# Performance work log

Hardware: AMD Instinct MI355X
Metric: run time of the kernel (lower is better)

The kernel has to match this reference:

```python
import jax, jax.numpy as jnp
import numpy as np

N = 50000      # nodes
E = 800000     # edges (before self loops)
EMB = 128      # input feature dim
HID = 32       # per-head hidden dim
HEADS = 4      # gat1 heads
G = 64         # graphs in batch
NEG_SLOPE = 0.2


def setup_inputs() -> dict:
    key = jax.random.key(0)
    ks = jax.random.split(key, 14)
    glorot = lambda k, shape, fan: (jax.random.normal(k, shape) / np.sqrt(fan)).astype(jnp.float32)
    x = jax.random.normal(ks[0], (N, EMB), dtype=jnp.float32)
    edge_index = jax.random.randint(ks[1], (2, E), 0, N, dtype=jnp.int64)
    batch = jnp.sort(jax.random.randint(ks[2], (N,), 0, G, dtype=jnp.int64))
    return {
        "x": x,
        "edge_index": edge_index,
        "batch": batch,
        # GATConv 1: EMB -> HID per head, HEADS heads, concat
        "W1": glorot(ks[3], (EMB, HEADS * HID), EMB),
        "att_src1": glorot(ks[4], (HEADS, HID), HID),
        "att_dst1": glorot(ks[5], (HEADS, HID), HID),
        "b1": jnp.zeros((HEADS * HID,), jnp.float32),
        # GATConv 2: HEADS*HID -> HID, 1 head
        "W2": glorot(ks[6], (HEADS * HID, HID), HEADS * HID),
        "att_src2": glorot(ks[7], (1, HID), HID),
        "att_dst2": glorot(ks[8], (1, HID), HID),
        "b2": jnp.zeros((HID,), jnp.float32),
        # attentional pooling gate MLP: Linear(HID,HID)->ReLU->Linear(HID,1)
        "g_w1": glorot(ks[9], (HID, HID), HID),
        "g_b1": jnp.zeros((HID,), jnp.float32),
        "g_w2": glorot(ks[10], (HID, 1), HID),
        "g_b2": jnp.zeros((1,), jnp.float32),
    }


def _gat(x, W, att_src, att_dst, bias, src, dst, heads, out_dim):
    """PyG-style GATConv with precomputed self-looped (src, dst)."""
    n = x.shape[0]
    h = (x @ W).reshape(n, heads, out_dim)              # [N, H, C]
    a_src = (h * att_src).sum(-1)                       # [N, H]
    a_dst = (h * att_dst).sum(-1)                       # [N, H]
    e = jax.nn.leaky_relu(a_src[src] + a_dst[dst], NEG_SLOPE)   # [Etot, H]
    # segment softmax over incoming edges of each dst node
    m = jax.ops.segment_max(e, dst, num_segments=n)
    ex = jnp.exp(e - m[dst])
    denom = jax.ops.segment_sum(ex, dst, num_segments=n)
    alpha = ex / (denom[dst] + 1e-16)                   # [Etot, H]
    out = jax.ops.segment_sum(alpha[:, :, None] * h[src], dst, num_segments=n)
    return out.reshape(n, heads * out_dim) + bias


def reference(x, edge_index, batch, W1, att_src1, att_dst1, b1,
              W2, att_src2, att_dst2, b2, g_w1, g_b1, g_w2, g_b2):
    n = x.shape[0]
    loops = jnp.arange(n, dtype=edge_index.dtype)
    src = jnp.concatenate([edge_index[0], loops])       # add_self_loops=True
    dst = jnp.concatenate([edge_index[1], loops])
    h = jax.nn.elu(_gat(x, W1, att_src1, att_dst1, b1, src, dst, HEADS, HID))
    h = jax.nn.elu(_gat(h, W2, att_src2, att_dst2, b2, src, dst, 1, HID))
    # attentional aggregation per graph
    gate = jax.nn.relu(h @ g_w1 + g_b1) @ g_w2 + g_b2   # [N, 1]
    gm = jax.ops.segment_max(gate, batch, num_segments=G)
    ge = jnp.exp(gate - gm[batch])
    gs = jax.ops.segment_sum(ge, batch, num_segments=G)
    w = ge / (gs[batch] + 1e-16)
    return jax.ops.segment_sum(w * h, batch, num_segments=G)  # [G, HID]
```

## Files before the change

kernel.cpp:

```cpp
#include <hip/hip_runtime.h>
#include <hip/hip_bf16.h>

#define NEG_SLOPE 0.2f
#define BW  128
#define BSH 7

__device__ __forceinline__ float elu1f(float v) {
    return v > 0.f ? v : expm1f(v);
}
__device__ __forceinline__ float bf2f(ushort u) {
    return __uint_as_float(((unsigned)u) << 16);
}
__device__ __forceinline__ ushort f2bf(float f) {
    return __bfloat16_as_ushort(__float2bfloat16(f));
}
__device__ __forceinline__ unsigned fflip(float f) {
    unsigned u = __float_as_uint(f);
    return (u & 0x80000000u) ? ~u : (u | 0x80000000u);
}
__device__ __forceinline__ float funflip(unsigned u) {
    u = (u & 0x80000000u) ? (u & 0x7FFFFFFFu) : ~u;
    return __uint_as_float(u);
}

__global__ __launch_bounds__(256) void k_bcount(
    const int* __restrict__ ei, int E, int Et, int nbk, int* __restrict__ bcnt)
{
    __shared__ int h[512];
    for (int i = threadIdx.x; i < nbk; i += 256) h[i] = 0;
    __syncthreads();
    const int start = blockIdx.x * 4096;
    const int end   = min(start + 4096, Et);
    for (int i = start + threadIdx.x; i < end; i += 256) {
        int d = (i < E) ? ei[E + i] : i - E;
        atomicAdd(&h[d >> BSH], 1);
    }
    __syncthreads();
    for (int i = threadIdx.x; i < nbk; i += 256)
        if (h[i]) atomicAdd(&bcnt[i], h[i]);
}

__global__ __launch_bounds__(512) void k_bscan(
    const int* __restrict__ bcnt, int nbk, int Et,
    int* __restrict__ bbase, int* __restrict__ bcur)
{
    __shared__ int s[512];
    int v = (threadIdx.x < nbk) ? bcnt[threadIdx.x] : 0;
    s[threadIdx.x] = v;
    __syncthreads();
#pragma unroll
    for (int off = 1; off < 512; off <<= 1) {
        int t = (threadIdx.x >= off) ? s[threadIdx.x - off] : 0;
        __syncthreads();
        s[threadIdx.x] += t;
        __syncthreads();
    }
    if (threadIdx.x < nbk) {
        int ex = s[threadIdx.x] - v;
        bbase[threadIdx.x] = ex;
        bcur[threadIdx.x]  = ex;
    }
    if (threadIdx.x == 0) bbase[nbk] = Et;
}

__global__ __launch_bounds__(256) void k_bscatter(
    const int* __restrict__ ei, int E, int Et, int nbk,
    int* __restrict__ bcur, int2* __restrict__ ebuk)
{
    __shared__ int h[512];
    __shared__ int cur[512];
    for (int i = threadIdx.x; i < nbk; i += 256) h[i] = 0;
    __syncthreads();
    const int start = blockIdx.x * 4096;
    const int end   = min(start + 4096, Et);
    for (int i = start + threadIdx.x; i < end; i += 256) {
        int d = (i < E) ? ei[E + i] : i - E;
        atomicAdd(&h[d >> BSH], 1);
    }
    __syncthreads();
    for (int i = threadIdx.x; i < nbk; i += 256)
        cur[i] = h[i] ? atomicAdd(&bcur[i], h[i]) : 0;
    __syncthreads();
    for (int i = start + threadIdx.x; i < end; i += 256) {
        int s, d;
        if (i < E) { s = ei[i]; d = ei[E + i]; } else { s = i - E; d = s; }
        int p = atomicAdd(&cur[d >> BSH], 1);
        ebuk[p] = make_int2(s, d);
    }
}

__global__ __launch_bounds__(256) void k_bdeg(
    const int2* __restrict__ ebuk, const int* __restrict__ bbase,
    int N, int* __restrict__ deg)
{
    const int b = blockIdx.x;
    __shared__ int cnt[BW];
    if (threadIdx.x < BW) cnt[threadIdx.x] = 0;
    __syncthreads();
    const int d0 = b << BSH;
    const int e0 = bbase[b], e1 = bbase[b + 1];
    for (int i = e0 + threadIdx.x; i < e1; i += 256)
        atomicAdd(&cnt[ebuk[i].y - d0], 1);
    __syncthreads();
    if (threadIdx.x < BW) {
        int d = d0 + threadIdx.x;
        if (d < N) deg[d] = cnt[threadIdx.x];
    }
}

__global__ __launch_bounds__(256) void k_fine(
    const int2* __restrict__ ebuk, const int* __restrict__ bbase,
    const int* __restrict__ rowp, int N, int* __restrict__ esrc)
{
    const int b = blockIdx.x;
    __shared__ int lcur[BW];
    const int d0 = b << BSH;
    if (threadIdx.x < BW) {
        int d = d0 + threadIdx.x;
        lcur[threadIdx.x] = (d < N) ? rowp[d] : 0;
    }
    __syncthreads();
    const int e0 = bbase[b], e1 = bbase[b + 1];
    for (int i = e0 + threadIdx.x; i < e1; i += 256) {
        int2 e = ebuk[i];
        int p = atomicAdd(&lcur[e.y - d0], 1);
        esrc[p] = e.x;
    }
}

__global__ __launch_bounds__(256) void k_scan1(const int* __restrict__ deg, int N,
                                               int* __restrict__ row, int* __restrict__ bsum)
{
    __shared__ int s[256];
    int i = blockIdx.x * 256 + threadIdx.x;
    int v = (i < N) ? deg[i] : 0;
    s[threadIdx.x] = v;
    __syncthreads();
#pragma unroll
    for (int off = 1; off < 256; off <<= 1) {
        int t = (threadIdx.x >= off) ? s[threadIdx.x - off] : 0;
        __syncthreads();
        s[threadIdx.x] += t;
        __syncthreads();
    }
    if (i < N) row[i] = s[threadIdx.x] - v;
    if (threadIdx.x == 255) bsum[blockIdx.x] = s[255];
}

__global__ __launch_bounds__(256) void k_scan2(int* __restrict__ bsum, int nb)
{
    __shared__ int s[256];
    int v = (threadIdx.x < nb) ? bsum[threadIdx.x] : 0;
    s[threadIdx.x] = v;
    __syncthreads();
#pragma unroll
    for (int off = 1; off < 256; off <<= 1) {
        int t = (threadIdx.x >= off) ? s[threadIdx.x - off] : 0;
        __syncthreads();
        s[threadIdx.x] += t;
        __syncthreads();
    }
    if (threadIdx.x < nb) bsum[threadIdx.x] = s[threadIdx.x] - v;
}

__global__ void k_scan3(int* __restrict__ row, const int* __restrict__ bsum, int N, int Et)
{
    int i = blockIdx.x * 256 + threadIdx.x;
    if (i < N) row[i] += bsum[blockIdx.x];
    if (i == 0) row[N] = Et;
}

template <int H>
__global__ __launch_bounds__(256) void k_redmax(const unsigned* __restrict__ in, int nblk,
                                                float* __restrict__ out)
{
    __shared__ unsigned sm[H];
    if (threadIdx.x < H) sm[threadIdx.x] = 0;
    __syncthreads();
    unsigned m[H];
#pragma unroll
    for (int h = 0; h < H; h++) m[h] = 0;
    for (int i = threadIdx.x; i < nblk; i += 256) {
#pragma unroll
        for (int h = 0; h < H; h++) m[h] = max(m[h], in[i * H + h]);
    }
#pragma unroll
    for (int h = 0; h < H; h++) atomicMax(&sm[h], m[h]);
    __syncthreads();
    if (threadIdx.x < H) out[threadIdx.x] = funflip(sm[threadIdx.x]);
}

__global__ __launch_bounds__(256) void k_gemm1(
    const float* __restrict__ x, const float* __restrict__ W,
    const float* __restrict__ att_s, const float* __restrict__ att_d,
    ushort* __restrict__ h1, float* __restrict__ as1, float* __restrict__ ad1,
    unsigned* __restrict__ blkmax, int N)
{
    __shared__ __align__(16) float sW[16][128];
    __shared__ __align__(16) float sX[32][16];
    __shared__ unsigned smax[4];
    const int t  = threadIdx.x;
    const int c4 = t & 31;
    const int rg = t >> 5;
    const int row0 = blockIdx.x * 32;
    const float4* W4 = (const float4*)W;

    if (t < 4) smax[t] = 0;

    float4 acc[4];
#pragma unroll
    for (int i = 0; i < 4; i++) acc[i] = {0.f, 0.f, 0.f, 0.f};

    for (int k0 = 0; k0 < 128; k0 += 16) {
        __syncthreads();
#pragma unroll
        for (int j = 0; j < 2; j++) {
            int idx = j * 256 + t;
            int r = idx >> 5, cc = idx & 31;
            *(float4*)&sW[r][cc * 4] = W4[(k0 + r) * 32 + cc];
        }
        if (t < 128) {
            int r = t >> 2, q = t & 3;
            int row = row0 + r;
            float4 v = {0.f, 0.f, 0.f, 0.f};
            if (row < N) v = *(const float4*)&x[(long long)row * 128 + k0 + q * 4];
            *(float4*)&sX[r][q * 4] = v;
        }
        __syncthreads();
#pragma unroll
        for (int g = 0; g < 4; g++) {
            const int kk = g * 4;
            const float4 w0 = *(const float4*)&sW[kk + 0][c4 * 4];
            const float4 w1 = *(const float4*)&sW[kk + 1][c4 * 4];
            const float4 w2 = *(const float4*)&sW[kk + 2][c4 * 4];
            const float4 w3 = *(const float4*)&sW[kk + 3][c4 * 4];
#pragma unroll
            for (int i = 0; i < 4; i++) {
                const float4 xv = *(const float4*)&sX[rg * 4 + i][kk];
                acc[i].x = fmaf(xv.x, w0.x, acc[i].x);
                acc[i].y = fmaf(xv.x, w0.y, acc[i].y);
                acc[i].z = fmaf(xv.x, w0.z, acc[i].z);
                acc[i].w = fmaf(xv.x, w0.w, acc[i].w);
                acc[i].x = fmaf(xv.y, w1.x, acc[i].x);
                acc[i].y = fmaf(xv.y, w1.y, acc[i].y);
                acc[i].z = fmaf(xv.y, w1.z, acc[i].z);
                acc[i].w = fmaf(xv.y, w1.w, acc[i].w);
                acc[i].x = fmaf(xv.z, w2.x, acc[i].x);
                acc[i].y = fmaf(xv.z, w2.y, acc[i].y);
                acc[i].z = fmaf(xv.z, w2.z, acc[i].z);
                acc[i].w = fmaf(xv.z, w2.w, acc[i].w);
                acc[i].x = fmaf(xv.w, w3.x, acc[i].x);
                acc[i].y = fmaf(xv.w, w3.y, acc[i].y);
                acc[i].z = fmaf(xv.w, w3.z, acc[i].z);
                acc[i].w = fmaf(xv.w, w3.w, acc[i].w);
            }
        }
    }

    const float4 avs = *(const float4*)&att_s[c4 * 4];
    const float4 avd = *(const float4*)&att_d[c4 * 4];
    const int hd = c4 >> 3;
    float lmax = -INFINITY;
#pragma unroll
    for (int i = 0; i < 4; i++) {
        int row = row0 + rg * 4 + i;
        if (row < N) {
            ushort4 hb;
            hb.x = f2bf(acc[i].x); hb.y = f2bf(acc[i].y);
            hb.z = f2bf(acc[i].z); hb.w = f2bf(acc[i].w);
            *(ushort4*)&h1[(long long)row * 128 + c4 * 4] = hb;
            float s = acc[i].x * avs.x + acc[i].y * avs.y + acc[i].z * avs.z + acc[i].w * avs.w;
            float d = acc[i].x * avd.x + acc[i].y * avd.y + acc[i].z * avd.z + acc[i].w * avd.w;
#pragma unroll
            for (int off = 4; off > 0; off >>= 1) {
                s += __shfl_xor(s, off, 64);
                d += __shfl_xor(d, off, 64);
            }
            if ((c4 & 7) == 0) {
                as1[row * 4 + hd] = s; ad1[row * 4 + hd] = d;
                lmax = fmaxf(lmax, s);
            }
        }
    }
    if ((c4 & 7) == 0) atomicMax(&smax[hd], fflip(lmax));
    __syncthreads();
    if (t < 4) blkmax[blockIdx.x * 4 + t] = smax[t];
}

__global__ __launch_bounds__(256) void k_gemm2(
    const float* __restrict__ xin, const float* __restrict__ W,
    const float* __restrict__ b1,
    const float* __restrict__ att_s, const float* __restrict__ att_d,
    ushort* __restrict__ h2, float* __restrict__ as2, float* __restrict__ ad2,
    unsigned* __restrict__ blkmax, int N)
{
    __shared__ __align__(16) float sW[16][32];
    __shared__ __align__(16) float sX[128][16];
    __shared__ unsigned smax1;
    const int t  = threadIdx.x;
    const int c4 = t & 7;
    const int rg = t >> 3;
    const int row0 = blockIdx.x * 128;
    const float4* W4 = (const float4*)W;

    if (t == 0) smax1 = 0;

    float4 acc[4];
#pragma unroll
    for (int i = 0; i < 4; i++) acc[i] = {0.f, 0.f, 0.f, 0.f};

    for (int k0 = 0; k0 < 128; k0 += 16) {
        __syncthreads();
        if (t < 128) {
            int r = t >> 3, cc = t & 7;
            *(float4*)&sW[r][cc * 4] = W4[(k0 + r) * 8 + cc];
        }
#pragma unroll
        for (int j = 0; j < 2; j++) {
            int idx = j * 256 + t;
            int r = idx >> 2, q = idx & 3;
            int row = row0 + r;
            float4 v = {0.f, 0.f, 0.f, 0.f};
            if (row < N) {
                v = *(const float4*)&xin[(long long)row * 128 + k0 + q * 4];
                float4 b = *(const float4*)&b1[k0 + q * 4];
                v.x = elu1f(v.x + b.x); v.y = elu1f(v.y + b.y);
                v.z = elu1f(v.z + b.z); v.w = elu1f(v.w + b.w);
            }
            *(float4*)&sX[r][q * 4] = v;
        }
        __syncthreads();
#pragma unroll
        for (int g = 0; g < 4; g++) {
            const int kk = g * 4;
            const float4 w0 = *(const float4*)&sW[kk + 0][c4 * 4];
            const float4 w1 = *(const float4*)&sW[kk + 1][c4 * 4];
            const float4 w2 = *(const float4*)&sW[kk + 2][c4 * 4];
            const float4 w3 = *(const float4*)&sW[kk + 3][c4 * 4];
#pragma unroll
            for (int i = 0; i < 4; i++) {
                const float4 xv = *(const float4*)&sX[rg * 4 + i][kk];
                acc[i].x = fmaf(xv.x, w0.x, acc[i].x);
                acc[i].y = fmaf(xv.x, w0.y, acc[i].y);
                acc[i].z = fmaf(xv.x, w0.z, acc[i].z);
                acc[i].w = fmaf(xv.x, w0.w, acc[i].w);
                acc[i].x = fmaf(xv.y, w1.x, acc[i].x);
                acc[i].y = fmaf(xv.y, w1.y, acc[i].y);
                acc[i].z = fmaf(xv.y, w1.z, acc[i].z);
                acc[i].w = fmaf(xv.y, w1.w, acc[i].w);
                acc[i].x = fmaf(xv.z, w2.x, acc[i].x);
                acc[i].y = fmaf(xv.z, w2.y, acc[i].y);
                acc[i].z = fmaf(xv.z, w2.z, acc[i].z);
                acc[i].w = fmaf(xv.z, w2.w, acc[i].w);
                acc[i].x = fmaf(xv.w, w3.x, acc[i].x);
                acc[i].y = fmaf(xv.w, w3.y, acc[i].y);
                acc[i].z = fmaf(xv.w, w3.z, acc[i].z);
                acc[i].w = fmaf(xv.w, w3.w, acc[i].w);
            }
        }
    }

    const float4 avs = *(const float4*)&att_s[c4 * 4];
    const float4 avd = *(const float4*)&att_d[c4 * 4];
    float lmax = -INFINITY;
#pragma unroll
    for (int i = 0; i < 4; i++) {
        int row = row0 + rg * 4 + i;
        if (row < N) {
            ushort4 hb;
            hb.x = f2bf(acc[i].x); hb.y = f2bf(acc[i].y);
            hb.z = f2bf(acc[i].z); hb.w = f2bf(acc[i].w);
            *(ushort4*)&h2[(long long)row * 32 + c4 * 4] = hb;
            float s = acc[i].x * avs.x + acc[i].y * avs.y + acc[i].z * avs.z + acc[i].w * avs.w;
            float d = acc[i].x * avd.x + acc[i].y * avd.y + acc[i].z * avd.z + acc[i].w * avd.w;
#pragma unroll
            for (int off = 4; off > 0; off >>= 1) {
                s += __shfl_xor(s, off, 64);
                d += __shfl_xor(d, off, 64);
            }
            if (c4 == 0) {
                as2[row] = s; ad2[row] = d;
                lmax = fmaxf(lmax, s);
            }
        }
    }
    if (c4 == 0) atomicMax(&smax1, fflip(lmax));
    __syncthreads();
    if (t == 0) blkmax[blockIdx.x] = smax1;
}

__global__ __launch_bounds__(256) void k_agg1(
    const int* __restrict__ row, const int* __restrict__ esrc,
    const float* __restrict__ as, const float* __restrict__ ad,
    const float* __restrict__ gmaxh,
    const ushort* __restrict__ h,
    float* __restrict__ out, int N)
{
    const int lane = threadIdx.x & 63;
    const int wid  = threadIdx.x >> 6;
    const int n = blockIdx.x * 4 + wid;
    if (n >= N) return;
    const int e0 = row[n], e1 = row[n + 1];

    const float4 ad4 = *(const float4*)&ad[n * 4];
    const int half = lane >> 5;
    const int l    = lane & 31;
    const int hd   = l >> 3;
    const float adh = hd == 0 ? ad4.x : hd == 1 ? ad4.y : hd == 2 ? ad4.z : ad4.w;
    float mh = gmaxh[hd] + adh;
    mh = mh >= 0.f ? mh : NEG_SLOPE * mh;

    const unsigned lofs = (unsigned)(l * 4);
    float4 acc = {0.f, 0.f, 0.f, 0.f};
    float wsum = 0.f;
    for (int base = e0; base < e1; base += 8) {
        const int eA = base + half,     eB = base + 2 + half;
        const int eC = base + 4 + half, eD = base + 6 + half;
        const bool vA = eA < e1, vB = eB < e1, vC = eC < e1, vD = eD < e1;
        const int sA = vA ? esrc[eA] : 0;
        const int sB = vB ? esrc[eB] : 0;
        const int sC = vC ? esrc[eC] : 0;
        const int sD = vD ? esrc[eD] : 0;
        const float4 aA = *(const float4*)&as[sA * 4];
        const float4 aB = *(const float4*)&as[sB * 4];
        const float4 aC = *(const float4*)&as[sC * 4];
        const float4 aD = *(const float4*)&as[sD * 4];
        const ushort4 hA = *(const ushort4*)&h[(unsigned)sA * 128u + lofs];
        const ushort4 hB = *(const ushort4*)&h[(unsigned)sB * 128u + lofs];
        const ushort4 hC = *(const ushort4*)&h[(unsigned)sC * 128u + lofs];
        const ushort4 hD = *(const ushort4*)&h[(unsigned)sD * 128u + lofs];

        float evA = (hd == 0 ? aA.x : hd == 1 ? aA.y : hd == 2 ? aA.z : aA.w) + adh;
        evA = evA >= 0.f ? evA : NEG_SLOPE * evA;
        const float wA = vA ? __expf(evA - mh) : 0.f;
        float evB = (hd == 0 ? aB.x : hd == 1 ? aB.y : hd == 2 ? aB.z : aB.w) + adh;
        evB = evB >= 0.f ? evB : NEG_SLOPE * evB;
        const float wB = vB ? __expf(evB - mh) : 0.f;
        float evC = (hd == 0 ? aC.x : hd == 1 ? aC.y : hd == 2 ? aC.z : aC.w) + adh;
        evC = evC >= 0.f ? evC : NEG_SLOPE * evC;
        const float wC = vC ? __expf(evC - mh) : 0.f;
        float evD = (hd == 0 ? aD.x : hd == 1 ? aD.y : hd == 2 ? aD.z : aD.w) + adh;
        evD = evD >= 0.f ? evD : NEG_SLOPE * evD;
        const float wD = vD ? __expf(evD - mh) : 0.f;

        acc.x = fmaf(wA, bf2f(hA.x), acc.x);
        acc.y = fmaf(wA, bf2f(hA.y), acc.y);
        acc.z = fmaf(wA, bf2f(hA.z), acc.z);
        acc.w = fmaf(wA, bf2f(hA.w), acc.w);
        acc.x = fmaf(wB, bf2f(hB.x), acc.x);
        acc.y = fmaf(wB, bf2f(hB.y), acc.y);
        acc.z = fmaf(wB, bf2f(hB.z), acc.z);
        acc.w = fmaf(wB, bf2f(hB.w), acc.w);
        acc.x = fmaf(wC, bf2f(hC.x), acc.x);
        acc.y = fmaf(wC, bf2f(hC.y), acc.y);
        acc.z = fmaf(wC, bf2f(hC.z), acc.z);
        acc.w = fmaf(wC, bf2f(hC.w), acc.w);
        acc.x = fmaf(wD, bf2f(hD.x), acc.x);
        acc.y = fmaf(wD, bf2f(hD.y), acc.y);
        acc.z = fmaf(wD, bf2f(hD.z), acc.z);
        acc.w = fmaf(wD, bf2f(hD.w), acc.w);
        wsum += (wA + wB) + (wC + wD);
    }
    acc.x += __shfl_xor(acc.x, 32, 64);
    acc.y += __shfl_xor(acc.y, 32, 64);
    acc.z += __shfl_xor(acc.z, 32, 64);
    acc.w += __shfl_xor(acc.w, 32, 64);
    wsum  += __shfl_xor(wsum, 32, 64);

    if (half == 0) {
        const float inv = 1.f / (wsum + 1e-16f);
        float4 o; o.x = acc.x * inv; o.y = acc.y * inv; o.z = acc.z * inv; o.w = acc.w * inv;
        *(float4*)&out[(long long)n * 128 + l * 4] = o;
    }
}

__global__ __launch_bounds__(256) void k_agg2(
    const int* __restrict__ row, const int* __restrict__ esrc,
    const float* __restrict__ as, const float* __restrict__ ad,
    const float* __restrict__ gmax2,
    const ushort* __restrict__ h,
    float* __restrict__ out, int N)
{
    const int lane = threadIdx.x & 63;
    const int wid  = threadIdx.x >> 6;
    const int n = blockIdx.x * 4 + wid;
    if (n >= N) return;
    const int e0 = row[n], e1 = row[n + 1];
    const float adv = ad[n];
    float m = gmax2[0] + adv;
    m = m >= 0.f ? m : NEG_SLOPE * m;

    const int g  = lane >> 3;
    const int l8 = lane & 7;
    const unsigned lofs = (unsigned)(l8 * 4);
    float4 acc = {0.f, 0.f, 0.f, 0.f};
    float wsum = 0.f;
    for (int base = e0; base < e1; base += 32) {
        const int eA = base + g,      eB = base + 8 + g;
        const int eC = base + 16 + g, eD = base + 24 + g;
        const bool vA = eA < e1, vB = eB < e1, vC = eC < e1, vD = eD < e1;
        const int sA = vA ? esrc[eA] : 0;
        const int sB = vB ? esrc[eB] : 0;
        const int sC = vC ? esrc[eC] : 0;
        const int sD = vD ? esrc[eD] : 0;
        const float asA = as[sA], asB = as[sB], asC = as[sC], asD = as[sD];
        const ushort4 hA = *(const ushort4*)&h[(unsigned)sA * 32u + lofs];
        const ushort4 hB = *(const ushort4*)&h[(unsigned)sB * 32u + lofs];
        const ushort4 hC = *(const ushort4*)&h[(unsigned)sC * 32u + lofs];
        const ushort4 hD = *(const ushort4*)&h[(unsigned)sD * 32u + lofs];

        float evA = asA + adv; evA = evA >= 0.f ? evA : NEG_SLOPE * evA;
        const float wA = vA ? __expf(evA - m) : 0.f;
        float evB = asB + adv; evB = evB >= 0.f ? evB : NEG_SLOPE * evB;
        const float wB = vB ? __expf(evB - m) : 0.f;
        float evC = asC + adv; evC = evC >= 0.f ? evC : NEG_SLOPE * evC;
        const float wC = vC ? __expf(evC - m) : 0.f;
        float evD = asD + adv; evD = evD >= 0.f ? evD : NEG_SLOPE * evD;
        const float wD = vD ? __expf(evD - m) : 0.f;

        acc.x = fmaf(wA, bf2f(hA.x), acc.x);
        acc.y = fmaf(wA, bf2f(hA.y), acc.y);
        acc.z = fmaf(wA, bf2f(hA.z), acc.z);
        acc.w = fmaf(wA, bf2f(hA.w), acc.w);
        acc.x = fmaf(wB, bf2f(hB.x), acc.x);
        acc.y = fmaf(wB, bf2f(hB.y), acc.y);
        acc.z = fmaf(wB, bf2f(hB.z), acc.z);
        acc.w = fmaf(wB, bf2f(hB.w), acc.w);
        acc.x = fmaf(wC, bf2f(hC.x), acc.x);
        acc.y = fmaf(wC, bf2f(hC.y), acc.y);
        acc.z = fmaf(wC, bf2f(hC.z), acc.z);
        acc.w = fmaf(wC, bf2f(hC.w), acc.w);
        acc.x = fmaf(wD, bf2f(hD.x), acc.x);
        acc.y = fmaf(wD, bf2f(hD.y), acc.y);
        acc.z = fmaf(wD, bf2f(hD.z), acc.z);
        acc.w = fmaf(wD, bf2f(hD.w), acc.w);
        wsum += (wA + wB) + (wC + wD);
    }
#pragma unroll
    for (int off = 8; off < 64; off <<= 1) {
        acc.x += __shfl_xor(acc.x, off, 64);
        acc.y += __shfl_xor(acc.y, off, 64);
        acc.z += __shfl_xor(acc.z, off, 64);
        acc.w += __shfl_xor(acc.w, off, 64);
        wsum  += __shfl_xor(wsum, off, 64);
    }
    if (lane < 8) {
        const float inv = 1.f / (wsum + 1e-16f);
        float4 o; o.x = acc.x * inv; o.y = acc.y * inv; o.z = acc.z * inv; o.w = acc.w * inv;
        *(float4*)&out[(long long)n * 32 + lane * 4] = o;
    }
}

__global__ __launch_bounds__(256) void k_gate(
    const float* __restrict__ out2, const float* __restrict__ b2,
    const float* __restrict__ gw1, const float* __restrict__ gb1,
    const float* __restrict__ gw2, const float* __restrict__ gb2,
    float* __restrict__ gate, int N)
{
    const int c = threadIdx.x & 31, grp = threadIdx.x >> 5;
    const int n = blockIdx.x * 8 + grp;
    if (n >= N) return;
    float v = out2[(long long)n * 32 + c] + b2[c];
    v = elu1f(v);
    float t1 = gb1[c];
#pragma unroll
    for (int k = 0; k < 32; k++) {
        float hk = __shfl(v, k, 32);
        t1 = fmaf(hk, gw1[k * 32 + c], t1);
    }
    t1 = fmaxf(t1, 0.f);
    float gv = t1 * gw2[c];
#pragma unroll
    for (int off = 16; off > 0; off >>= 1) gv += __shfl_xor(gv, off, 32);
    if (c == 0) gate[n] = gv + gb2[0];
}

__global__ __launch_bounds__(128) void k_bounds(
    const int* __restrict__ batch, int* __restrict__ gbound, int N, int G)
{
    int t = threadIdx.x;
    if (t > G) return;
    int lo = 0, hi = N;
    while (lo < hi) { int mid = (lo + hi) >> 1; if (batch[mid] < t) lo = mid + 1; else hi = mid; }
    gbound[t] = lo;
}

__global__ __launch_bounds__(256) void k_gmax(
    const float* __restrict__ gate, const int* __restrict__ gbound,
    unsigned* __restrict__ gmax)
{
    const int g  = blockIdx.x >> 3;
    const int ch = blockIdx.x & 7;
    const int s0 = gbound[g], s1 = gbound[g + 1];
    const int len = s1 - s0;
    const int c0 = s0 + (int)(((long long)len * ch) >> 3);
    const int c1 = s0 + (int)(((long long)len * (ch + 1)) >> 3);

    __shared__ float sred[4];
    float m = -INFINITY;
    for (int n = c0 + threadIdx.x; n < c1; n += 256) m = fmaxf(m, gate[n]);
#pragma unroll
    for (int off = 32; off > 0; off >>= 1) m = fmaxf(m, __shfl_xor(m, off, 64));
    if ((threadIdx.x & 63) == 0) sred[threadIdx.x >> 6] = m;
    __syncthreads();
    if (threadIdx.x == 0) {
        m = fmaxf(fmaxf(sred[0], sred[1]), fmaxf(sred[2], sred[3]));
        atomicMax(&gmax[g], fflip(m));
    }
}

__global__ __launch_bounds__(256) void k_pool3(
    const float* __restrict__ out2, const float* __restrict__ b2,
    const float* __restrict__ gate, const int* __restrict__ gbound,
    const unsigned* __restrict__ gmax, float* __restrict__ partials)
{
    const int g  = blockIdx.x >> 3;
    const int ch = blockIdx.x & 7;
    const int s0 = gbound[g], s1 = gbound[g + 1];
    const int len = s1 - s0;
    const int c0 = s0 + (int)(((long long)len * ch) >> 3);
    const int c1 = s0 + (int)(((long long)len * (ch + 1)) >> 3);

    const int c   = threadIdx.x & 31;
    const int grp = threadIdx.x >> 5;
    const float gm = funflip(gmax[g]);
    const float bc = b2[c];

    __shared__ float sacc[8][32];
    __shared__ float swsum[8];

    float acc = 0.f, wsum = 0.f;
    for (int n = c0 + grp; n < c1; n += 8) {
        float v = elu1f(out2[(long long)n * 32 + c] + bc);
        float ge = __expf(gate[n] - gm);
        acc = fmaf(ge, v, acc);
        wsum += ge;
    }
    sacc[grp][c] = acc;
    if (c == 0) swsum[grp] = wsum;
    __syncthreads();

    if (grp == 0) {
        float a = 0.f, wtot = 0.f;
#pragma unroll
        for (int i = 0; i < 8; i++) { a += sacc[i][c]; wtot += swsum[i]; }
        partials[(long long)blockIdx.x * 33 + c] = a;
        if (c == 0) partials[(long long)blockIdx.x * 33 + 32] = wtot;
    }
}

__global__ __launch_bounds__(256) void k_pool4(
    const float* __restrict__ partials, float* __restrict__ out)
{
    const int g   = blockIdx.x;
    const int c   = threadIdx.x & 31;
    const int p   = threadIdx.x >> 5;

    __shared__ float sacc[8][32];
    __shared__ float swsum[8];

    sacc[p][c] = partials[(long long)(g * 8 + p) * 33 + c];
    if (c == 0) swsum[p] = partials[(long long)(g * 8 + p) * 33 + 32];
    __syncthreads();

    if (p == 0) {
        float a = 0.f, wtot = 0.f;
#pragma unroll
        for (int i = 0; i < 8; i++) { a += sacc[i][c]; wtot += swsum[i]; }
        out[g * 32 + c] = a / (wtot + 1e-16f);
    }
}

extern "C" void kernel_launch(void* const* d_in, const int* in_sizes, int n_in,
                              void* d_out, int out_size, void* d_ws, size_t ws_size,
                              hipStream_t stream)
{
    const float* x    = (const float*)d_in[0];
    const int*   ei   = (const int*)d_in[1];
    const int*   batch= (const int*)d_in[2];
    const float* W1   = (const float*)d_in[3];
    const float* as1w = (const float*)d_in[4];
    const float* ad1w = (const float*)d_in[5];
    const float* b1   = (const float*)d_in[6];
    const float* W2   = (const float*)d_in[7];
    const float* as2w = (const float*)d_in[8];
    const float* ad2w = (const float*)d_in[9];
    const float* b2   = (const float*)d_in[10];
    const float* gw1  = (const float*)d_in[11];
    const float* gb1  = (const float*)d_in[12];
    const float* gw2  = (const float*)d_in[13];
    const float* gb2  = (const float*)d_in[14];

    const int N  = in_sizes[2];
    const int E  = in_sizes[1] / 2;
    const int Et = E + N;
    const int nb = (N + 255) / 256;
    const int G  = 64;
    const int nbk   = (N + BW - 1) >> BSH;
    const int nchk  = (Et + 4095) / 4096;
    const int nblk1 = (N + 31) / 32;
    const int nblk2 = (N + 127) / 128;

    float* ws = (float*)d_ws;
    size_t o = 0;
    int2*  ebuk = (int2*)(ws + o); o += (size_t)Et * 2;
    ushort* h1 = (ushort*)(ws + o); o += (size_t)N * 64;
    float* out1 = ws + o; o += (size_t)N * 128;
    ushort* h2 = (ushort*)(ws + o); o += (size_t)N * 16;
    float* out2 = ws + o; o += (size_t)N * 32;
    float* a_s1 = ws + o; o += (size_t)N * 4;
    float* a_d1 = ws + o; o += (size_t)N * 4;
    float* a_s2 = ws + o; o += (size_t)N;
    float* a_d2 = ws + o; o += (size_t)N;
    float* gate = ws + o; o += (size_t)N;
    int*   deg  = (int*)(ws + o); o += (size_t)N;
    int*   rowp = (int*)(ws + o); o += (size_t)N + 1;
    int*   esrc = (int*)(ws + o); o += (size_t)Et;
    int*   bsum = (int*)(ws + o); o += 256;
    int*   bbase= (int*)(ws + o); o += (size_t)nbk + 1;
    int*   bcur = (int*)(ws + o); o += (size_t)nbk;
    int*   gbound = (int*)(ws + o); o += G + 1;
    float* partials = ws + o; o += (size_t)G * 8 * 33;
    unsigned* blkmax1 = (unsigned*)(ws + o); o += (size_t)nblk1 * 4;
    unsigned* blkmax2 = (unsigned*)(ws + o); o += (size_t)nblk2;
    float* gmaxh = ws + o; o += 4;
    float* gmax2 = ws + o; o += 4;
    size_t zstart = o;
    int*      bcnt = (int*)(ws + o); o += (size_t)nbk;
    unsigned* gmax = (unsigned*)(ws + o); o += G;
    size_t zbytes = (o - zstart) * sizeof(float);

    hipMemsetAsync(ws + zstart, 0, zbytes, stream);

    k_bcount  <<<nchk, 256, 0, stream>>>(ei, E, Et, nbk, bcnt);
    k_bscan   <<<1, 512, 0, stream>>>(bcnt, nbk, Et, bbase, bcur);
    k_bscatter<<<nchk, 256, 0, stream>>>(ei, E, Et, nbk, bcur, ebuk);
    k_bdeg    <<<nbk, 256, 0, stream>>>(ebuk, bbase, N, deg);
    k_scan1   <<<nb, 256, 0, stream>>>(deg, N, rowp, bsum);
    k_scan2   <<<1, 256, 0, stream>>>(bsum, nb);
    k_scan3   <<<nb, 256, 0, stream>>>(rowp, bsum, N, Et);
    k_fine    <<<nbk, 256, 0, stream>>>(ebuk, bbase, rowp, N, esrc);
    k_bounds  <<<1, 128, 0, stream>>>(batch, gbound, N, G);

    k_gemm1<<<nblk1, 256, 0, stream>>>(x, W1, as1w, ad1w, h1, a_s1, a_d1, blkmax1, N);
    k_redmax<4><<<1, 256, 0, stream>>>(blkmax1, nblk1, gmaxh);
    k_agg1 <<<(N + 3) / 4, 256, 0, stream>>>(rowp, esrc, a_s1, a_d1, gmaxh, h1, out1, N);

    k_gemm2<<<nblk2, 256, 0, stream>>>(out1, W2, b1, as2w, ad2w, h2, a_s2, a_d2, blkmax2, N);
    k_redmax<1><<<1, 256, 0, stream>>>(blkmax2, nblk2, gmax2);
    k_agg2 <<<(N + 3) / 4, 256, 0, stream>>>(rowp, esrc, a_s2, a_d2, gmax2, h2, out2, N);

    k_gate <<<(N + 7) / 8, 256, 0, stream>>>(out2, b2, gw1, gb1, gw2, gb2, gate, N);
    k_gmax <<<G * 8, 256, 0, stream>>>(gate, gbound, gmax);
    k_pool3<<<G * 8, 256, 0, stream>>>(out2, b2, gate, gbound, gmax, partials);
    k_pool4<<<G, 256, 0, stream>>>(partials, (float*)d_out);
}
```

Baseline: 228.3 us.

## Fuse CSR degree, scan and fill into one bucket kernel; transpose layer-1 source scores

Merges the per-bucket degree count, the three-kernel global prefix scan and the fine scatter into a single k_csr kernel. Each block derives its row offsets from the bucket base plus a local shared-memory scan, which removes four launches and the deg/bsum round trips. Separately, layer-1 source attention scores are stored head-major, so each aggregation lane gathers one float for its head instead of a float4 and a select. The trade-off is uncoalesced strided writes in gemm1 and an extra barrier-heavy scan inside every bucket block.

Result: faster. 214.7 us (-6.0%).

```diff
diff --git a/kernel.cpp b/kernel.cpp
--- a/kernel.cpp
+++ b/kernel.cpp
@@ -89,38 +89,38 @@
     }
 }
 
-__global__ __launch_bounds__(256) void k_bdeg(
+__global__ __launch_bounds__(256) void k_csr(
     const int2* __restrict__ ebuk, const int* __restrict__ bbase,
-    int N, int* __restrict__ deg)
+    int N, int Et, int* __restrict__ rowp, int* __restrict__ esrc)
 {
     const int b = blockIdx.x;
     __shared__ int cnt[BW];
+    __shared__ int pre[BW];
+    __shared__ int lcur[BW];
+    const int d0 = b << BSH;
     if (threadIdx.x < BW) cnt[threadIdx.x] = 0;
     __syncthreads();
-    const int d0 = b << BSH;
     const int e0 = bbase[b], e1 = bbase[b + 1];
     for (int i = e0 + threadIdx.x; i < e1; i += 256)
         atomicAdd(&cnt[ebuk[i].y - d0], 1);
     __syncthreads();
+    if (threadIdx.x < BW) pre[threadIdx.x] = cnt[threadIdx.x];
+    __syncthreads();
+#pragma unroll
+    for (int off = 1; off < BW; off <<= 1) {
+        int v = (threadIdx.x < BW && threadIdx.x >= off) ? pre[threadIdx.x - off] : 0;
+        __syncthreads();
+        if (threadIdx.x < BW) pre[threadIdx.x] += v;
+        __syncthreads();
+    }
     if (threadIdx.x < BW) {
+        int r = e0 + pre[threadIdx.x] - cnt[threadIdx.x];
         int d = d0 + threadIdx.x;
-        if (d < N) deg[d] = cnt[threadIdx.x];
-    }
-}
-
-__global__ __launch_bounds__(256) void k_fine(
-    const int2* __restrict__ ebuk, const int* __restrict__ bbase,
-    const int* __restrict__ rowp, int N, int* __restrict__ esrc)
-{
-    const int b = blockIdx.x;
-    __shared__ int lcur[BW];
-    const int d0 = b << BSH;
-    if (threadIdx.x < BW) {
-        int d = d0 + threadIdx.x;
-        lcur[threadIdx.x] = (d < N) ? rowp[d] : 0;
-    }
-    __syncthreads();
-    const int e0 = bbase[b], e1 = bbase[b + 1];
+        if (d < N) rowp[d] = r;
+        lcur[threadIdx.x] = r;
+    }
+    if (b == 0 && threadIdx.x == 0) rowp[N] = Et;
+    __syncthreads();
     for (int i = e0 + threadIdx.x; i < e1; i += 256) {
         int2 e = ebuk[i];
         int p = atomicAdd(&lcur[e.y - d0], 1);
@@ -128,48 +128,6 @@
     }
 }
 
-__global__ __launch_bounds__(256) void k_scan1(const int* __restrict__ deg, int N,
-                                               int* __restrict__ row, int* __restrict__ bsum)
-{
-    __shared__ int s[256];
-    int i = blockIdx.x * 256 + threadIdx.x;
-    int v = (i < N) ? deg[i] : 0;
-    s[threadIdx.x] = v;
-    __syncthreads();
-#pragma unroll
-    for (int off = 1; off < 256; off <<= 1) {
-        int t = (threadIdx.x >= off) ? s[threadIdx.x - off] : 0;
-        __syncthreads();
-        s[threadIdx.x] += t;
-        __syncthreads();
-    }
-    if (i < N) row[i] = s[threadIdx.x] - v;
-    if (threadIdx.x == 255) bsum[blockIdx.x] = s[255];
-}
-
-__global__ __launch_bounds__(256) void k_scan2(int* __restrict__ bsum, int nb)
-{
-    __shared__ int s[256];
-    int v = (threadIdx.x < nb) ? bsum[threadIdx.x] : 0;
-    s[threadIdx.x] = v;
-    __syncthreads();
-#pragma unroll
-    for (int off = 1; off < 256; off <<= 1) {
-        int t = (threadIdx.x >= off) ? s[threadIdx.x - off] : 0;
-        __syncthreads();
-        s[threadIdx.x] += t;
-        __syncthreads();
-    }
-    if (threadIdx.x < nb) bsum[threadIdx.x] = s[threadIdx.x] - v;
-}
-
-__global__ void k_scan3(int* __restrict__ row, const int* __restrict__ bsum, int N, int Et)
-{
-    int i = blockIdx.x * 256 + threadIdx.x;
-    if (i < N) row[i] += bsum[blockIdx.x];
-    if (i == 0) row[N] = Et;
-}
-
 template <int H>
 __global__ __launch_bounds__(256) void k_redmax(const unsigned* __restrict__ in, int nblk,
                                                 float* __restrict__ out)
@@ -193,7 +151,7 @@
 __global__ __launch_bounds__(256) void k_gemm1(
     const float* __restrict__ x, const float* __restrict__ W,
     const float* __restrict__ att_s, const float* __restrict__ att_d,
-    ushort* __restrict__ h1, float* __restrict__ as1, float* __restrict__ ad1,
+    ushort* __restrict__ h1, float* __restrict__ asT, float* __restrict__ ad1,
     unsigned* __restrict__ blkmax, int N)
 {
     __shared__ __align__(16) float sW[16][128];
@@ -277,7 +235,8 @@
                 d += __shfl_xor(d, off, 64);
             }
             if ((c4 & 7) == 0) {
-                as1[row * 4 + hd] = s; ad1[row * 4 + hd] = d;
+                asT[(unsigned)hd * (unsigned)N + row] = s;
+                ad1[row * 4 + hd] = d;
                 lmax = fmaxf(lmax, s);
             }
         }
@@ -391,7 +350,7 @@
 
 __global__ __launch_bounds__(256) void k_agg1(
     const int* __restrict__ row, const int* __restrict__ esrc,
-    const float* __restrict__ as, const float* __restrict__ ad,
+    const float* __restrict__ asT, const float* __restrict__ ad,
     const float* __restrict__ gmaxh,
     const ushort* __restrict__ h,
     float* __restrict__ out, int N)
@@ -410,6 +369,7 @@
     float mh = gmaxh[hd] + adh;
     mh = mh >= 0.f ? mh : NEG_SLOPE * mh;
 
+    const float* asH = asT + (unsigned)hd * (unsigned)N;
     const unsigned lofs = (unsigned)(l * 4);
     float4 acc = {0.f, 0.f, 0.f, 0.f};
     float wsum = 0.f;
@@ -421,25 +381,25 @@
         const int sB = vB ? esrc[eB] : 0;
         const int sC = vC ? esrc[eC] : 0;
         const int sD = vD ? esrc[eD] : 0;
-        const float4 aA = *(const float4*)&as[sA * 4];
-        const float4 aB = *(const float4*)&as[sB * 4];
-        const float4 aC = *(const float4*)&as[sC * 4];
-        const float4 aD = *(const float4*)&as[sD * 4];
+        const float aA = asH[sA];
+        const float aB = asH[sB];
+        const float aC = asH[sC];
+        const float aD = asH[sD];
         const ushort4 hA = *(const ushort4*)&h[(unsigned)sA * 128u + lofs];
         const ushort4 hB = *(const ushort4*)&h[(unsigned)sB * 128u + lofs];
         const ushort4 hC = *(const ushort4*)&h[(unsigned)sC * 128u + lofs];
         const ushort4 hD = *(const ushort4*)&h[(unsigned)sD * 128u + lofs];
 
-        float evA = (hd == 0 ? aA.x : hd == 1 ? aA.y : hd == 2 ? aA.z : aA.w) + adh;
+        float evA = aA + adh;
         evA = evA >= 0.f ? evA : NEG_SLOPE * evA;
         const float wA = vA ? __expf(evA - mh) : 0.f;
-        float evB = (hd == 0 ? aB.x : hd == 1 ? aB.y : hd == 2 ? aB.z : aB.w) + adh;
+        float evB = aB + adh;
         evB = evB >= 0.f ? evB : NEG_SLOPE * evB;
         const float wB = vB ? __expf(evB - mh) : 0.f;
-        float evC = (hd == 0 ? aC.x : hd == 1 ? aC.y : hd == 2 ? aC.z : aC.w) + adh;
+        float evC = aC + adh;
         evC = evC >= 0.f ? evC : NEG_SLOPE * evC;
         const float wC = vC ? __expf(evC - mh) : 0.f;
-        float evD = (hd == 0 ? aD.x : hd == 1 ? aD.y : hd == 2 ? aD.z : aD.w) + adh;
+        float evD = aD + adh;
         evD = evD >= 0.f ? evD : NEG_SLOPE * evD;
         const float wD = vD ? __expf(evD - mh) : 0.f;
 
@@ -694,7 +654,6 @@
     const int N  = in_sizes[2];
     const int E  = in_sizes[1] / 2;
     const int Et = E + N;
-    const int nb = (N + 255) / 256;
     const int G  = 64;
     const int nbk   = (N + BW - 1) >> BSH;
     const int nchk  = (Et + 4095) / 4096;
@@ -708,15 +667,13 @@
     float* out1 = ws + o; o += (size_t)N * 128;
     ushort* h2 = (ushort*)(ws + o); o += (size_t)N * 16;
     float* out2 = ws + o; o += (size_t)N * 32;
-    float* a_s1 = ws + o; o += (size_t)N * 4;
+    float* asT1 = ws + o; o += (size_t)N * 4;
     float* a_d1 = ws + o; o += (size_t)N * 4;
     float* a_s2 = ws + o; o += (size_t)N;
     float* a_d2 = ws + o; o += (size_t)N;
     float* gate = ws + o; o += (size_t)N;
-    int*   deg  = (int*)(ws + o); o += (size_t)N;
     int*   rowp = (int*)(ws + o); o += (size_t)N + 1;
     int*   esrc = (int*)(ws + o); o += (size_t)Et;
-    int*   bsum = (int*)(ws + o); o += 256;
     int*   bbase= (int*)(ws + o); o += (size_t)nbk + 1;
     int*   bcur = (int*)(ws + o); o += (size_t)nbk;
     int*   gbound = (int*)(ws + o); o += G + 1;
@@ -735,16 +692,12 @@
     k_bcount  <<<nchk, 256, 0, stream>>>(ei, E, Et, nbk, bcnt);
     k_bscan   <<<1, 512, 0, stream>>>(bcnt, nbk, Et, bbase, bcur);
     k_bscatter<<<nchk, 256, 0, stream>>>(ei, E, Et, nbk, bcur, ebuk);
-    k_bdeg    <<<nbk, 256, 0, stream>>>(ebuk, bbase, N, deg);
-    k_scan1   <<<nb, 256, 0, stream>>>(deg, N, rowp, bsum);
-    k_scan2   <<<1, 256, 0, stream>>>(bsum, nb);
-    k_scan3   <<<nb, 256, 0, stream>>>(rowp, bsum, N, Et);
-    k_fine    <<<nbk, 256, 0, stream>>>(ebuk, bbase, rowp, N, esrc);
+    k_csr     <<<nbk, 256, 0, stream>>>(ebuk, bbase, N, Et, rowp, esrc);
     k_bounds  <<<1, 128, 0, stream>>>(batch, gbound, N, G);
 
-    k_gemm1<<<nblk1, 256, 0, stream>>>(x, W1, as1w, ad1w, h1, a_s1, a_d1, blkmax1, N);
+    k_gemm1<<<nblk1, 256, 0, stream>>>(x, W1, as1w, ad1w, h1, asT1, a_d1, blkmax1, N);
     k_redmax<4><<<1, 256, 0, stream>>>(blkmax1, nblk1, gmaxh);
-    k_agg1 <<<(N + 3) / 4, 256, 0, stream>>>(rowp, esrc, a_s1, a_d1, gmaxh, h1, out1, N);
+    k_agg1 <<<(N + 3) / 4, 256, 0, stream>>>(rowp, esrc, asT1, a_d1, gmaxh, h1, out1, N);
 
     k_gemm2<<<nblk2, 256, 0, stream>>>(out1, W2, b1, as2w, ad2w, h2, a_s2, a_d2, blkmax2, N);
     k_redmax<1><<<1, 256, 0, stream>>>(blkmax2, nblk2, gmax2);
```
